# Performance work log

Hardware: AMD Instinct MI355X
Metric: run time of the kernel (lower is better)

Reference implementation:

```python
import jax, jax.numpy as jnp
import numpy as np

N, E, D = 50000, 800000, 128   # nodes, edges, input feat dim
H, C = 4, 32                   # heads, per-head channels (H*C = 128)
OUT = 128                      # final linear out_channels
NEG_SLOPE = 0.2


def _glorot(k, shape):
    fan = shape[0] + shape[-1]
    return jax.random.normal(k, shape, jnp.float32) * np.float32(np.sqrt(2.0 / fan))


def setup_inputs() -> dict:
    key = jax.random.key(0)
    ks = jax.random.split(key, 16)
    HC = H * C
    z = lambda n: jnp.zeros((n,), jnp.float32)
    return {
        "x": jax.random.normal(ks[0], (N, D), jnp.float32),
        "edge_index": jax.random.randint(ks[1], (2, E), 0, N),
        "edge_attr": jax.random.uniform(ks[2], (E, 1), jnp.float32),
        # GATv2 layer 1 (in = D)
        "Wl1": _glorot(ks[3], (D, HC)), "bl1": z(HC),
        "Wr1": _glorot(ks[4], (D, HC)), "br1": z(HC),
        "We1": _glorot(ks[5], (1, HC)),
        "att1": _glorot(ks[6], (H, C)),
        "bo1": z(HC),
        # GATv2 layer 2 (in = H*C)
        "Wl2": _glorot(ks[7], (HC, HC)), "bl2": z(HC),
        "Wr2": _glorot(ks[8], (HC, HC)), "br2": z(HC),
        "We2": _glorot(ks[9], (1, HC)),
        "att2": _glorot(ks[10], (H, C)),
        "bo2": z(HC),
        # final Linear
        "Wlin": _glorot(ks[11], (HC, OUT)), "blin": z(OUT),
    }


def _segment_softmax(logits, seg, n):
    # logits: [E_tot, H], seg: [E_tot] target node ids
    m = jax.ops.segment_max(logits, seg, num_segments=n)          # [N, H]
    m = jnp.where(jnp.isfinite(m), m, 0.0)                         # empty-segment guard
    e = jnp.exp(logits - m[seg])
    s = jax.ops.segment_sum(e, seg, num_segments=n)                # [N, H]
    return e / (s[seg] + 1e-16)


def _gatv2_layer(x, src, dst, eattr, Wl, bl, Wr, br, We, att, bo):
    n = x.shape[0]
    xl = (x @ Wl + bl).reshape(n, H, C)   # source transform (lin_l)
    xr = (x @ Wr + br).reshape(n, H, C)   # target transform (lin_r)
    ee = (eattr @ We).reshape(-1, H, C)   # edge transform (lin_edge)
    m = jax.nn.leaky_relu(xl[src] + xr[dst] + ee, NEG_SLOPE)       # [E_tot, H, C]
    logits = jnp.einsum('ehc,hc->eh', m, att)                      # [E_tot, H]
    alpha = _segment_softmax(logits, dst, n)                       # [E_tot, H]
    out = jax.ops.segment_sum(xl[src] * alpha[..., None], dst, num_segments=n)
    return out.reshape(n, H * C) + bo


def _with_self_loops(edge_index, edge_attr, n):
    # PyG add_self_loops(fill_value='mean'): loop attr = mean of incoming edge attrs
    src, dst = edge_index[0], edge_index[1]
    sums = jax.ops.segment_sum(edge_attr, dst, num_segments=n)     # [N, 1]
    cnts = jax.ops.segment_sum(jnp.ones((edge_attr.shape[0], 1), edge_attr.dtype),
                               dst, num_segments=n)
    loop_attr = jnp.where(cnts > 0, sums / jnp.maximum(cnts, 1.0), 0.0)
    ar = jnp.arange(n, dtype=src.dtype)
    full_src = jnp.concatenate([src, ar])
    full_dst = jnp.concatenate([dst, ar])
    full_attr = jnp.concatenate([edge_attr, loop_attr], axis=0)
    return full_src, full_dst, full_attr


def reference(x, edge_index, edge_attr,
              Wl1, bl1, Wr1, br1, We1, att1, bo1,
              Wl2, bl2, Wr2, br2, We2, att2, bo2,
              Wlin, blin):
    x = x.astype(jnp.float32)
    edge_attr = edge_attr.astype(jnp.float32)
    src, dst, eattr = _with_self_loops(edge_index, edge_attr, x.shape[0])
    h = jax.nn.relu(_gatv2_layer(x, src, dst, eattr, Wl1, bl1, Wr1, br1, We1, att1, bo1))
    h = jax.nn.relu(_gatv2_layer(h, src, dst, eattr, Wl2, bl2, Wr2, br2, We2, att2, bo2))
    return jax.nn.relu(h @ Wlin + blin)
```

## Files before the change

### kernel.cpp

```cpp
#include <hip/hip_runtime.h>
#include <hip/hip_fp16.h>
#include <math.h>

#define NEG 0.2f
#define CNT_SHIFT 42
#define SUM_MASK ((1ULL << CNT_SHIFT) - 1)
#define ROWS 48

typedef _Float16 hf2 __attribute__((ext_vector_type(2)));
typedef _Float16 hf8 __attribute__((ext_vector_type(8)));
typedef float f4 __attribute__((ext_vector_type(4)));

template <int CTRL>
__device__ __forceinline__ float dpp_radd(float x) {
  int t = __builtin_amdgcn_update_dpp(0, __float_as_int(x), CTRL, 0xf, 0xf,
                                      false);
  return x + __int_as_float(t);
}

__global__ __launch_bounds__(256) void k_prep(const int* __restrict__ ei,
    const float* __restrict__ eattr, unsigned long long* __restrict__ hist,
    unsigned* __restrict__ edge, int E, const float* __restrict__ W0,
    const float* __restrict__ W1, const float* __restrict__ W2,
    const float* __restrict__ W3, const float* __restrict__ W4,
    uint4* __restrict__ wout, int nbH) {
  int bid = blockIdx.x;
  int tid = threadIdx.x;
  if (bid < nbH) {
    int e = bid * 256 + tid;
    if (e >= E) return;
    int d = ei[E + e];
    int src = ei[e];
    float ea = eattr[e];
    unsigned long long fx = (unsigned long long)(ea * 4294967296.0f);
    unsigned long long old = atomicAdd(&hist[d], (1ULL << CNT_SHIFT) + fx);
    int rank = (int)(old >> CNT_SHIFT);
    _Float16 h = (_Float16)ea;
    unsigned hb = (unsigned)__builtin_bit_cast(unsigned short, h);
    if (rank < ROWS)
      edge[(size_t)d * ROWS + rank] = (unsigned)src | (hb << 16);
  } else {
    int gid = (bid - nbH) * 256 + tid;
    if (gid >= 5 * 2048) return;
    int mat = gid >> 11;
    int line = gid & 2047;
    const float* W = mat == 0 ? W0 : mat == 1 ? W1 : mat == 2 ? W2
                   : mat == 3 ? W3 : W4;
    int lane = line & 63;
    int nt = (line >> 6) & 7;
    int kc = line >> 9;
    int kbase = kc * 32 + (lane >> 4) * 8;
    int col = nt * 16 + (lane & 15);
    hf8 h;
#pragma unroll
    for (int j = 0; j < 8; ++j)
      h[j] = (_Float16)W[(size_t)(kbase + j) * 128 + col];
    wout[gid] = __builtin_bit_cast(uint4, h);
  }
}

template <int NMAT, int F32IN, int HALF_OUT>
__global__ __launch_bounds__(256, 1) void k_gemm4(
    const void* __restrict__ Xv, const uint4* __restrict__ Wp0,
    const uint4* __restrict__ Wp1, const float* __restrict__ B0,
    const float* __restrict__ B1, void* __restrict__ Y0v,
    void* __restrict__ Y1v, int nrows, int dorelu) {
  __shared__ uint4 Wl[NMAT * 2048];
  int tid = threadIdx.x;
  for (int i = tid; i < 2048; i += 256) Wl[i] = Wp0[i];
  if (NMAT == 2)
    for (int i = tid; i < 2048; i += 256) Wl[2048 + i] = Wp1[i];

  int lane = tid & 63, wid = tid >> 6;
  int quad = lane >> 4, rl = lane & 15;
  int rbase = blockIdx.x * 256 + wid * 64;

  hf8 a[4][4];
#pragma unroll
  for (int rs = 0; rs < 4; ++rs) {
    int gr = rbase + rs * 16 + rl;
    gr = gr < nrows ? gr : nrows - 1;
    if (F32IN) {
      const float* xp = (const float*)Xv + (size_t)gr * 128 + quad * 8;
#pragma unroll
      for (int kc = 0; kc < 4; ++kc) {
        float4 u = *reinterpret_cast<const float4*>(xp + kc * 32);
        float4 w2 = *reinterpret_cast<const float4*>(xp + kc * 32 + 4);
        uint4 pk;
        pk.x = __builtin_bit_cast(unsigned, __builtin_amdgcn_cvt_pkrtz(u.x, u.y));
        pk.y = __builtin_bit_cast(unsigned, __builtin_amdgcn_cvt_pkrtz(u.z, u.w));
        pk.z = __builtin_bit_cast(unsigned, __builtin_amdgcn_cvt_pkrtz(w2.x, w2.y));
        pk.w = __builtin_bit_cast(unsigned, __builtin_amdgcn_cvt_pkrtz(w2.z, w2.w));
        a[kc][rs] = __builtin_bit_cast(hf8, pk);
      }
    } else {
      const _Float16* xp = (const _Float16*)Xv + (size_t)gr * 128 + quad * 8;
#pragma unroll
      for (int kc = 0; kc < 4; ++kc)
        a[kc][rs] = *reinterpret_cast<const hf8*>(xp + kc * 32);
    }
  }

  f4 acc[NMAT][4][8];
#pragma unroll
  for (int m = 0; m < NMAT; ++m)
#pragma unroll
    for (int rs = 0; rs < 4; ++rs)
#pragma unroll
      for (int nt = 0; nt < 8; ++nt) acc[m][rs][nt] = (f4)0.f;

  __syncthreads();

#pragma unroll
  for (int kc = 0; kc < 4; ++kc) {
#pragma unroll
    for (int nt = 0; nt < 8; ++nt) {
#pragma unroll
      for (int m = 0; m < NMAT; ++m) {
        hf8 w = __builtin_bit_cast(hf8,
            Wl[m * 2048 + (kc * 8 + nt) * 64 + lane]);
#pragma unroll
        for (int rs = 0; rs < 4; ++rs)
          acc[m][rs][nt] = __builtin_amdgcn_mfma_f32_16x16x32_f16(
              w, a[kc][rs], acc[m][rs][nt], 0, 0, 0);
      }
    }
  }

#pragma unroll
  for (int m = 0; m < NMAT; ++m) {
    const float* Bb = m ? B1 : B0;
    void* Yv = m ? Y1v : Y0v;
#pragma unroll
    for (int rs = 0; rs < 4; ++rs) {
      int row = rbase + rs * 16 + rl;
      if (row < nrows) {
#pragma unroll
        for (int nt = 0; nt < 8; ++nt) {
          f4 av = acc[m][rs][nt];
          int col = nt * 16 + quad * 4;
          float4 bb = *reinterpret_cast<const float4*>(&Bb[col]);
          float o0 = av[0] + bb.x, o1 = av[1] + bb.y;
          float o2 = av[2] + bb.z, o3 = av[3] + bb.w;
          if (dorelu) {
            o0 = fmaxf(o0, 0.f); o1 = fmaxf(o1, 0.f);
            o2 = fmaxf(o2, 0.f); o3 = fmaxf(o3, 0.f);
          }
          if (HALF_OUT) {
            unsigned p0 = __builtin_bit_cast(unsigned,
                __builtin_amdgcn_cvt_pkrtz(o0, o1));
            unsigned p1 = __builtin_bit_cast(unsigned,
                __builtin_amdgcn_cvt_pkrtz(o2, o3));
            *reinterpret_cast<uint2*>((_Float16*)Yv + (size_t)row * 128 + col)
                = make_uint2(p0, p1);
          } else {
            *reinterpret_cast<float4*>((float*)Yv + (size_t)row * 128 + col)
                = make_float4(o0, o1, o2, o3);
          }
        }
      }
    }
  }
}

__global__ __launch_bounds__(256) void k_gat(const hf2* __restrict__ xl,
    const hf2* __restrict__ xr, const unsigned* __restrict__ edge,
    const unsigned long long* __restrict__ hist, const float* __restrict__ We,
    const float* __restrict__ att, const float* __restrict__ bo,
    hf2* __restrict__ out, int n) {
  int lane = threadIdx.x & 63;
  int wid = threadIdx.x >> 6;
  int v = blockIdx.x * 4 + wid;
  if (v >= n) return;
  int ch = lane * 2;
  hf2 weh = {(_Float16)We[ch], (_Float16)We[ch + 1]};
  hf2 atth = {(_Float16)(att[ch] * 1.44269504f),
              (_Float16)(att[ch + 1] * 1.44269504f)};
  hf2 negh = {(_Float16)NEG, (_Float16)NEG};
  hf2 xrh = xr[(size_t)v * 64 + lane];
  unsigned long long hv = hist[v];
  int cnt = (int)(hv >> CNT_SHIFT);
  int cntc = cnt < ROWS ? cnt : ROWS;
  const unsigned* erow = edge + (size_t)v * ROWS;

  float denom[2] = {0.f, 0.f};
  float ac0[2] = {0.f, 0.f}, ac1[2] = {0.f, 0.f};

  int full = cntc & ~7;
  for (int ofs = 0; ofs < full; ofs += 8) {
    const unsigned* ep = erow + ofs;
    unsigned rec[8];
#pragma unroll
    for (int j = 0; j < 8; ++j) rec[j] = ep[j];
    hf2 xv[8];
#pragma unroll
    for (int j = 0; j < 8; ++j)
      xv[j] = xl[(size_t)(rec[j] & 0xffffu) * 64 + lane];
    float p[8];
#pragma unroll
    for (int j = 0; j < 8; ++j) {
      hf2 eah = __builtin_bit_cast(hf2, (rec[j] >> 16) * 0x10001u);
      hf2 t = (xv[j] + xrh) + eah * weh;
      hf2 tn = t * negh;
      t = __builtin_elementwise_max(t, tn);
      p[j] = __builtin_amdgcn_fdot2(t, atth, 0.f, false);
    }
#pragma unroll
    for (int j = 0; j < 8; ++j) {
      p[j] = dpp_radd<0xB1>(p[j]);
      p[j] = dpp_radd<0x4E>(p[j]);
      p[j] = dpp_radd<0x141>(p[j]);
      p[j] = dpp_radd<0x140>(p[j]);
    }
#pragma unroll
    for (int j = 0; j < 8; ++j) {
      float w = __builtin_amdgcn_exp2f(p[j]);
      denom[j & 1] += w;
      ac0[j & 1] = fmaf(w, (float)xv[j].x, ac0[j & 1]);
      ac1[j & 1] = fmaf(w, (float)xv[j].y, ac1[j & 1]);
    }
  }
  if (full < cntc) {
    const unsigned* ep = erow + full;
    unsigned rec[8];
#pragma unroll
    for (int j = 0; j < 8; ++j) rec[j] = ep[j];
    hf2 xv[8];
#pragma unroll
    for (int j = 0; j < 8; ++j) {
      unsigned si = rec[j] & 0xffffu;
      si = si < (unsigned)n ? si : 0u;
      xv[j] = xl[(size_t)si * 64 + lane];
    }
    float p[8];
#pragma unroll
    for (int j = 0; j < 8; ++j) {
      hf2 eah = __builtin_bit_cast(hf2, (rec[j] >> 16) * 0x10001u);
      hf2 t = (xv[j] + xrh) + eah * weh;
      hf2 tn = t * negh;
      t = __builtin_elementwise_max(t, tn);
      p[j] = __builtin_amdgcn_fdot2(t, atth, 0.f, false);
    }
#pragma unroll
    for (int j = 0; j < 8; ++j) {
      p[j] = dpp_radd<0xB1>(p[j]);
      p[j] = dpp_radd<0x4E>(p[j]);
      p[j] = dpp_radd<0x141>(p[j]);
      p[j] = dpp_radd<0x140>(p[j]);
    }
#pragma unroll
    for (int j = 0; j < 8; ++j) {
      float w = (full + j < cntc) ? __builtin_amdgcn_exp2f(p[j]) : 0.f;
      denom[j & 1] += w;
      ac0[j & 1] = fmaf(w, (float)xv[j].x, ac0[j & 1]);
      ac1[j & 1] = fmaf(w, (float)xv[j].y, ac1[j & 1]);
    }
  }
  {
    float sumf = (float)(hv & SUM_MASK) * 2.3283064365386963e-10f;
    float mean = cnt > 0 ? sumf / (float)cnt : 0.f;
    hf2 xself = xl[(size_t)v * 64 + lane];
    _Float16 mh = (_Float16)mean;
    hf2 meanh = {mh, mh};
    hf2 t = (xself + xrh) + meanh * weh;
    hf2 tn = t * negh;
    t = __builtin_elementwise_max(t, tn);
    float ps = __builtin_amdgcn_fdot2(t, atth, 0.f, false);
    ps = dpp_radd<0xB1>(ps);
    ps = dpp_radd<0x4E>(ps);
    ps = dpp_radd<0x141>(ps);
    ps = dpp_radd<0x140>(ps);
    float w = __builtin_amdgcn_exp2f(ps);
    denom[0] += w;
    ac0[0] = fmaf(w, (float)xself.x, ac0[0]);
    ac1[0] = fmaf(w, (float)xself.y, ac1[0]);
  }
  float rden = 1.0f / (denom[0] + denom[1] + 1e-16f);
  float o0 = fmaxf(fmaf(ac0[0] + ac0[1], rden, bo[ch]), 0.f);
  float o1 = fmaxf(fmaf(ac1[0] + ac1[1], rden, bo[ch + 1]), 0.f);
  hf2 oh = {(_Float16)o0, (_Float16)o1};
  out[(size_t)v * 64 + lane] = oh;
}

extern "C" void kernel_launch(void* const* d_in, const int* in_sizes, int n_in,
                              void* d_out, int out_size, void* d_ws, size_t ws_size,
                              hipStream_t stream) {
  const float* x     = (const float*)d_in[0];
  const int*   ei    = (const int*)d_in[1];
  const float* eattr = (const float*)d_in[2];
  const float* Wl1 = (const float*)d_in[3];
  const float* bl1 = (const float*)d_in[4];
  const float* Wr1 = (const float*)d_in[5];
  const float* br1 = (const float*)d_in[6];
  const float* We1 = (const float*)d_in[7];
  const float* att1 = (const float*)d_in[8];
  const float* bo1 = (const float*)d_in[9];
  const float* Wl2 = (const float*)d_in[10];
  const float* bl2 = (const float*)d_in[11];
  const float* Wr2 = (const float*)d_in[12];
  const float* br2 = (const float*)d_in[13];
  const float* We2 = (const float*)d_in[14];
  const float* att2 = (const float*)d_in[15];
  const float* bo2 = (const float*)d_in[16];
  const float* Wlin = (const float*)d_in[17];
  const float* blin = (const float*)d_in[18];
  float* out = (float*)d_out;

  const int N = in_sizes[0] / 128;
  const int E = in_sizes[1] / 2;

  hf2* xl = (hf2*)d_ws;
  hf2* xr = xl + (size_t)N * 64;
  hf2* h16 = xr + (size_t)N * 64;
  uint4* w16 = (uint4*)(h16 + (size_t)N * 64);
  unsigned long long* hist = (unsigned long long*)(w16 + 5 * 2048);
  unsigned* edge = (unsigned*)(hist + N);

  (void)hipMemsetAsync(hist, 0, sizeof(unsigned long long) * (size_t)N,
                       stream);

  int nbH = (E + 255) / 256;
  int gGat = (N + 3) / 4;
  int gGemm = (N + 255) / 256;

  k_prep<<<nbH + 40, 256, 0, stream>>>(ei, eattr, hist, edge, E,
      Wl1, Wr1, Wl2, Wr2, Wlin, w16, nbH);

  k_gemm4<2, 1, 1><<<gGemm, 256, 0, stream>>>(x, w16, w16 + 2048,
      bl1, br1, xl, xr, N, 0);
  k_gat<<<gGat, 256, 0, stream>>>(xl, xr, edge, hist, We1, att1, bo1, h16, N);

  k_gemm4<2, 0, 1><<<gGemm, 256, 0, stream>>>(h16, w16 + 2 * 2048,
      w16 + 3 * 2048, bl2, br2, xl, xr, N, 0);
  k_gat<<<gGat, 256, 0, stream>>>(xl, xr, edge, hist, We2, att2, bo2, h16, N);

  k_gemm4<1, 0, 0><<<gGemm, 256, 0, stream>>>(h16, w16 + 4 * 2048, nullptr,
      blin, nullptr, out, nullptr, N, 1);
}
```

Before: 309.5 us.

## Fuse edge prep and weight packing into first GEMM launch, halve GEMM row tiles

Merges the edge histogram/bucketing pass, the layer-2 and final weight packing, and the layer-1 GEMM into one heterogeneous kernel. The layer-1 GEMM blocks pack their fp32 weights into LDS directly instead of reading a pre-packed buffer. This removes one launch and the serial dependency between prep and the first GEMM. GEMM tiles shrink from 256 to 128 rows per block with two blocks per CU, trading weight reloads per block for more occupancy and more blocks. Edge prep now handles 8 edges per thread to raise memory-level parallelism.

```diff
diff --git a/kernel.cpp b/kernel.cpp
--- a/kernel.cpp
+++ b/kernel.cpp
@@ -18,50 +18,153 @@
   return x + __int_as_float(t);
 }
 
-__global__ __launch_bounds__(256) void k_prep(const int* __restrict__ ei,
+__device__ __forceinline__ uint4 pack_wline(const float* __restrict__ W,
+                                            int L) {
+  int lane = L & 63, nt = (L >> 6) & 7, kc = L >> 9;
+  int kbase = kc * 32 + (lane >> 4) * 8;
+  int col = nt * 16 + (lane & 15);
+  const float* wp = W + (size_t)kbase * 128 + col;
+  uint4 pk;
+  pk.x = __builtin_bit_cast(unsigned, __builtin_amdgcn_cvt_pkrtz(wp[0], wp[128]));
+  pk.y = __builtin_bit_cast(unsigned, __builtin_amdgcn_cvt_pkrtz(wp[256], wp[384]));
+  pk.z = __builtin_bit_cast(unsigned, __builtin_amdgcn_cvt_pkrtz(wp[512], wp[640]));
+  pk.w = __builtin_bit_cast(unsigned, __builtin_amdgcn_cvt_pkrtz(wp[768], wp[896]));
+  return pk;
+}
+
+__global__ __launch_bounds__(256, 2) void k_fuse1(
+    const float* __restrict__ X, const float* __restrict__ Wa,
+    const float* __restrict__ Wb, const float* __restrict__ Ba,
+    const float* __restrict__ Bb, hf2* __restrict__ Y0, hf2* __restrict__ Y1,
+    int nrows, int gGemm, const int* __restrict__ ei,
     const float* __restrict__ eattr, unsigned long long* __restrict__ hist,
-    unsigned* __restrict__ edge, int E, const float* __restrict__ W0,
-    const float* __restrict__ W1, const float* __restrict__ W2,
-    const float* __restrict__ W3, const float* __restrict__ W4,
-    uint4* __restrict__ wout, int nbH) {
-  int bid = blockIdx.x;
-  int tid = threadIdx.x;
-  if (bid < nbH) {
-    int e = bid * 256 + tid;
-    if (e >= E) return;
-    int d = ei[E + e];
-    int src = ei[e];
-    float ea = eattr[e];
-    unsigned long long fx = (unsigned long long)(ea * 4294967296.0f);
-    unsigned long long old = atomicAdd(&hist[d], (1ULL << CNT_SHIFT) + fx);
-    int rank = (int)(old >> CNT_SHIFT);
-    _Float16 h = (_Float16)ea;
-    unsigned hb = (unsigned)__builtin_bit_cast(unsigned short, h);
-    if (rank < ROWS)
-      edge[(size_t)d * ROWS + rank] = (unsigned)src | (hb << 16);
+    unsigned* __restrict__ edge, int E, int nbP,
+    const float* __restrict__ W2a, const float* __restrict__ W2b,
+    const float* __restrict__ W2c, uint4* __restrict__ wout) {
+  __shared__ uint4 Wl[2][2048];
+  int bid = blockIdx.x, tid = threadIdx.x;
+
+  if (bid < gGemm) {
+#pragma unroll
+    for (int half = 0; half < 2; ++half) {
+      const float* W = half ? Wb : Wa;
+      for (int L = tid; L < 2048; L += 256) Wl[half][L] = pack_wline(W, L);
+    }
+
+    int lane = tid & 63, wid = tid >> 6;
+    int quad = lane >> 4, rl = lane & 15;
+    int rbase = bid * 128 + wid * 32;
+
+    hf8 a[4][2];
+#pragma unroll
+    for (int rs = 0; rs < 2; ++rs) {
+      int gr = rbase + rs * 16 + rl;
+      gr = gr < nrows ? gr : nrows - 1;
+      const float* xp = X + (size_t)gr * 128 + quad * 8;
+#pragma unroll
+      for (int kc = 0; kc < 4; ++kc) {
+        float4 u = *reinterpret_cast<const float4*>(xp + kc * 32);
+        float4 u2 = *reinterpret_cast<const float4*>(xp + kc * 32 + 4);
+        uint4 pk;
+        pk.x = __builtin_bit_cast(unsigned, __builtin_amdgcn_cvt_pkrtz(u.x, u.y));
+        pk.y = __builtin_bit_cast(unsigned, __builtin_amdgcn_cvt_pkrtz(u.z, u.w));
+        pk.z = __builtin_bit_cast(unsigned, __builtin_amdgcn_cvt_pkrtz(u2.x, u2.y));
+        pk.w = __builtin_bit_cast(unsigned, __builtin_amdgcn_cvt_pkrtz(u2.z, u2.w));
+        a[kc][rs] = __builtin_bit_cast(hf8, pk);
+      }
+    }
+
+    f4 acc[2][2][8];
+#pragma unroll
+    for (int m = 0; m < 2; ++m)
+#pragma unroll
+      for (int rs = 0; rs < 2; ++rs)
+#pragma unroll
+        for (int nt = 0; nt < 8; ++nt) acc[m][rs][nt] = (f4)0.f;
+
+    __syncthreads();
+
+#pragma unroll
+    for (int kc = 0; kc < 4; ++kc) {
+#pragma unroll
+      for (int nt = 0; nt < 8; ++nt) {
+#pragma unroll
+        for (int m = 0; m < 2; ++m) {
+          hf8 w = __builtin_bit_cast(hf8, Wl[m][(kc * 8 + nt) * 64 + lane]);
+          acc[m][0][nt] = __builtin_amdgcn_mfma_f32_16x16x32_f16(
+              w, a[kc][0], acc[m][0][nt], 0, 0, 0);
+          acc[m][1][nt] = __builtin_amdgcn_mfma_f32_16x16x32_f16(
+              w, a[kc][1], acc[m][1][nt], 0, 0, 0);
+        }
+      }
+    }
+
+#pragma unroll
+    for (int m = 0; m < 2; ++m) {
+      const float* Bb_ = m ? Bb : Ba;
+      hf2* Yv = m ? Y1 : Y0;
+#pragma unroll
+      for (int rs = 0; rs < 2; ++rs) {
+        int row = rbase + rs * 16 + rl;
+        if (row < nrows) {
+#pragma unroll
+          for (int nt = 0; nt < 8; ++nt) {
+            f4 av = acc[m][rs][nt];
+            int col = nt * 16 + quad * 4;
+            float4 bb = *reinterpret_cast<const float4*>(&Bb_[col]);
+            float o0 = av[0] + bb.x, o1 = av[1] + bb.y;
+            float o2 = av[2] + bb.z, o3 = av[3] + bb.w;
+            unsigned p0 = __builtin_bit_cast(unsigned,
+                __builtin_amdgcn_cvt_pkrtz(o0, o1));
+            unsigned p1 = __builtin_bit_cast(unsigned,
+                __builtin_amdgcn_cvt_pkrtz(o2, o3));
+            *reinterpret_cast<uint2*>((_Float16*)Yv + (size_t)row * 128 + col)
+                = make_uint2(p0, p1);
+          }
+        }
+      }
+    }
+  } else if (bid < gGemm + nbP) {
+    int e0 = (bid - gGemm) * 2048 + tid;
+    int d[8], s[8];
+    float ea[8];
+    bool valid[8];
+#pragma unroll
+    for (int j = 0; j < 8; ++j) {
+      int e = e0 + j * 256;
+      valid[j] = e < E;
+      int ec = valid[j] ? e : 0;
+      d[j] = ei[E + ec];
+      s[j] = ei[ec];
+      ea[j] = eattr[ec];
+    }
+#pragma unroll
+    for (int j = 0; j < 8; ++j) {
+      if (valid[j]) {
+        unsigned long long fx =
+            (unsigned long long)(ea[j] * 4294967296.0f);
+        unsigned long long old =
+            atomicAdd(&hist[d[j]], (1ULL << CNT_SHIFT) + fx);
+        int rank = (int)(old >> CNT_SHIFT);
+        _Float16 h = (_Float16)ea[j];
+        unsigned hb = (unsigned)__builtin_bit_cast(unsigned short, h);
+        if (rank < ROWS)
+          edge[(size_t)d[j] * ROWS + rank] = (unsigned)s[j] | (hb << 16);
+      }
+    }
   } else {
-    int gid = (bid - nbH) * 256 + tid;
-    if (gid >= 5 * 2048) return;
-    int mat = gid >> 11;
-    int line = gid & 2047;
-    const float* W = mat == 0 ? W0 : mat == 1 ? W1 : mat == 2 ? W2
-                   : mat == 3 ? W3 : W4;
-    int lane = line & 63;
-    int nt = (line >> 6) & 7;
-    int kc = line >> 9;
-    int kbase = kc * 32 + (lane >> 4) * 8;
-    int col = nt * 16 + (lane & 15);
-    hf8 h;
-#pragma unroll
-    for (int j = 0; j < 8; ++j)
-      h[j] = (_Float16)W[(size_t)(kbase + j) * 128 + col];
-    wout[gid] = __builtin_bit_cast(uint4, h);
-  }
-}
-
-template <int NMAT, int F32IN, int HALF_OUT>
-__global__ __launch_bounds__(256, 1) void k_gemm4(
-    const void* __restrict__ Xv, const uint4* __restrict__ Wp0,
+    int gid = (bid - gGemm - nbP) * 256 + tid;
+    if (gid < 3 * 2048) {
+      int mat = gid >> 11;
+      const float* W = mat == 0 ? W2a : mat == 1 ? W2b : W2c;
+      wout[gid] = pack_wline(W, gid & 2047);
+    }
+  }
+}
+
+template <int NMAT, int HALF_OUT>
+__global__ __launch_bounds__(256, 2) void k_gemm3(
+    const _Float16* __restrict__ X, const uint4* __restrict__ Wp0,
     const uint4* __restrict__ Wp1, const float* __restrict__ B0,
     const float* __restrict__ B1, void* __restrict__ Y0v,
     void* __restrict__ Y1v, int nrows, int dorelu) {
@@ -73,39 +176,24 @@
 
   int lane = tid & 63, wid = tid >> 6;
   int quad = lane >> 4, rl = lane & 15;
-  int rbase = blockIdx.x * 256 + wid * 64;
-
-  hf8 a[4][4];
-#pragma unroll
-  for (int rs = 0; rs < 4; ++rs) {
+  int rbase = blockIdx.x * 128 + wid * 32;
+
+  hf8 a[4][2];
+#pragma unroll
+  for (int rs = 0; rs < 2; ++rs) {
     int gr = rbase + rs * 16 + rl;
     gr = gr < nrows ? gr : nrows - 1;
-    if (F32IN) {
-      const float* xp = (const float*)Xv + (size_t)gr * 128 + quad * 8;
-#pragma unroll
-      for (int kc = 0; kc < 4; ++kc) {
-        float4 u = *reinterpret_cast<const float4*>(xp + kc * 32);
-        float4 w2 = *reinterpret_cast<const float4*>(xp + kc * 32 + 4);
-        uint4 pk;
-        pk.x = __builtin_bit_cast(unsigned, __builtin_amdgcn_cvt_pkrtz(u.x, u.y));
-        pk.y = __builtin_bit_cast(unsigned, __builtin_amdgcn_cvt_pkrtz(u.z, u.w));
-        pk.z = __builtin_bit_cast(unsigned, __builtin_amdgcn_cvt_pkrtz(w2.x, w2.y));
-        pk.w = __builtin_bit_cast(unsigned, __builtin_amdgcn_cvt_pkrtz(w2.z, w2.w));
-        a[kc][rs] = __builtin_bit_cast(hf8, pk);
-      }
-    } else {
-      const _Float16* xp = (const _Float16*)Xv + (size_t)gr * 128 + quad * 8;
-#pragma unroll
-      for (int kc = 0; kc < 4; ++kc)
-        a[kc][rs] = *reinterpret_cast<const hf8*>(xp + kc * 32);
-    }
-  }
-
-  f4 acc[NMAT][4][8];
+    const _Float16* xp = X + (size_t)gr * 128 + quad * 8;
+#pragma unroll
+    for (int kc = 0; kc < 4; ++kc)
+      a[kc][rs] = *reinterpret_cast<const hf8*>(xp + kc * 32);
+  }
+
+  f4 acc[NMAT][2][8];
 #pragma unroll
   for (int m = 0; m < NMAT; ++m)
 #pragma unroll
-    for (int rs = 0; rs < 4; ++rs)
+    for (int rs = 0; rs < 2; ++rs)
 #pragma unroll
       for (int nt = 0; nt < 8; ++nt) acc[m][rs][nt] = (f4)0.f;
 
@@ -119,10 +207,10 @@
       for (int m = 0; m < NMAT; ++m) {
         hf8 w = __builtin_bit_cast(hf8,
             Wl[m * 2048 + (kc * 8 + nt) * 64 + lane]);
-#pragma unroll
-        for (int rs = 0; rs < 4; ++rs)
-          acc[m][rs][nt] = __builtin_amdgcn_mfma_f32_16x16x32_f16(
-              w, a[kc][rs], acc[m][rs][nt], 0, 0, 0);
+        acc[m][0][nt] = __builtin_amdgcn_mfma_f32_16x16x32_f16(
+            w, a[kc][0], acc[m][0][nt], 0, 0, 0);
+        acc[m][1][nt] = __builtin_amdgcn_mfma_f32_16x16x32_f16(
+            w, a[kc][1], acc[m][1][nt], 0, 0, 0);
       }
     }
   }
@@ -132,7 +220,7 @@
     const float* Bb = m ? B1 : B0;
     void* Yv = m ? Y1v : Y0v;
 #pragma unroll
-    for (int rs = 0; rs < 4; ++rs) {
+    for (int rs = 0; rs < 2; ++rs) {
       int row = rbase + rs * 16 + rl;
       if (row < nrows) {
 #pragma unroll
@@ -313,27 +401,27 @@
   hf2* xr = xl + (size_t)N * 64;
   hf2* h16 = xr + (size_t)N * 64;
   uint4* w16 = (uint4*)(h16 + (size_t)N * 64);
-  unsigned long long* hist = (unsigned long long*)(w16 + 5 * 2048);
+  unsigned long long* hist = (unsigned long long*)(w16 + 3 * 2048);
   unsigned* edge = (unsigned*)(hist + N);
 
   (void)hipMemsetAsync(hist, 0, sizeof(unsigned long long) * (size_t)N,
                        stream);
 
-  int nbH = (E + 255) / 256;
+  int gGemm = (N + 127) / 128;
+  int nbP = (E + 2047) / 2048;
   int gGat = (N + 3) / 4;
-  int gGemm = (N + 255) / 256;
-
-  k_prep<<<nbH + 40, 256, 0, stream>>>(ei, eattr, hist, edge, E,
-      Wl1, Wr1, Wl2, Wr2, Wlin, w16, nbH);
-
-  k_gemm4<2, 1, 1><<<gGemm, 256, 0, stream>>>(x, w16, w16 + 2048,
-      bl1, br1, xl, xr, N, 0);
+
+  k_fuse1<<<gGemm + nbP + 24, 256, 0, stream>>>(x, Wl1, Wr1, bl1, br1,
+      xl, xr, N, gGemm, ei, eattr, hist, edge, E, nbP,
+      Wl2, Wr2, Wlin, w16);
+
   k_gat<<<gGat, 256, 0, stream>>>(xl, xr, edge, hist, We1, att1, bo1, h16, N);
 
-  k_gemm4<2, 0, 1><<<gGemm, 256, 0, stream>>>(h16, w16 + 2 * 2048,
-      w16 + 3 * 2048, bl2, br2, xl, xr, N, 0);
+  k_gemm3<2, 1><<<gGemm, 256, 0, stream>>>((const _Float16*)h16,
+      w16, w16 + 2048, bl2, br2, xl, xr, N, 0);
+
   k_gat<<<gGat, 256, 0, stream>>>(xl, xr, edge, hist, We2, att2, bo2, h16, N);
 
-  k_gemm4<1, 0, 0><<<gGemm, 256, 0, stream>>>(h16, w16 + 4 * 2048, nullptr,
-      blin, nullptr, out, nullptr, N, 1);
-}
+  k_gemm3<1, 0><<<gGemm, 256, 0, stream>>>((const _Float16*)h16,
+      w16 + 2 * 2048, nullptr, blin, nullptr, out, nullptr, N, 1);
+}
```

Measured after the change: 286.5 us. 7.4% less time.
